# Performance work log

Measured on AMD Instinct MI355X. Metric: run time of the kernel, lower is better.

Reference implementation:

```python
import jax, jax.numpy as jnp
import numpy as np

D_MODEL = 1024
D_FFN = 4096
N_HEAD = 16
D_K = D_MODEL // N_HEAD
EPS = 1e-10


def _layernorm(x, gamma, beta):
    mean = jnp.mean(x, axis=-1, keepdims=True)
    var = jnp.mean((x - mean) ** 2, axis=-1, keepdims=True)
    return gamma * ((x - mean) / jnp.sqrt(var + EPS)) + beta


def setup_inputs() -> dict:
    key = jax.random.key(0)
    ks = jax.random.split(key, 16)
    s = 1.0 / np.sqrt(D_MODEL)
    sf = 1.0 / np.sqrt(D_FFN)
    return {
        "x": jax.random.normal(ks[0], (4, 2048, D_MODEL), jnp.float32),
        "wq": jax.random.uniform(ks[1], (D_MODEL, D_MODEL), jnp.float32, -s, s),
        "bq": jnp.zeros((D_MODEL,), jnp.float32),
        "wk": jax.random.uniform(ks[2], (D_MODEL, D_MODEL), jnp.float32, -s, s),
        "bk": jnp.zeros((D_MODEL,), jnp.float32),
        "wv": jax.random.uniform(ks[3], (D_MODEL, D_MODEL), jnp.float32, -s, s),
        "bv": jnp.zeros((D_MODEL,), jnp.float32),
        "wo": jax.random.uniform(ks[4], (D_MODEL, D_MODEL), jnp.float32, -s, s),
        "bo": jnp.zeros((D_MODEL,), jnp.float32),
        "g1": jnp.ones((D_MODEL,), jnp.float32),
        "b1": jnp.zeros((D_MODEL,), jnp.float32),
        "w1": jax.random.uniform(ks[5], (D_MODEL, D_FFN), jnp.float32, -s, s),
        "bf1": jnp.zeros((D_FFN,), jnp.float32),
        "w2": jax.random.uniform(ks[6], (D_FFN, D_MODEL), jnp.float32, -sf, sf),
        "bf2": jnp.zeros((D_MODEL,), jnp.float32),
        "g2": jnp.ones((D_MODEL,), jnp.float32),
        "b2": jnp.zeros((D_MODEL,), jnp.float32),
    }


def reference(x, wq, bq, wk, bk, wv, bv, wo, bo, g1, b1, w1, bf1, w2, bf2, g2, b2):
    B, S, _ = x.shape
    # projections -> (B, H, S, d_k)
    q = (x @ wq + bq).reshape(B, S, N_HEAD, D_K).transpose(0, 2, 1, 3)
    k = (x @ wk + bk).reshape(B, S, N_HEAD, D_K).transpose(0, 2, 1, 3)
    v = (x @ wv + bv).reshape(B, S, N_HEAD, D_K).transpose(0, 2, 1, 3)
    score = jnp.einsum("bhqd,bhkd->bhqk", q, k) / jnp.sqrt(jnp.asarray(D_K, x.dtype))
    attn = jax.nn.softmax(score, axis=-1)
    out = jnp.einsum("bhqk,bhkd->bhqd", attn, v)
    out = out.transpose(0, 2, 1, 3).reshape(B, S, D_MODEL)
    out = out @ wo + bo
    out1 = _layernorm(x + out, g1, b1)
    # FFN (dropout is identity in eval mode)
    ff = jax.nn.relu(out1 @ w1 + bf1) @ w2 + bf2
    out2 = _layernorm(out1 + ff, g2, b2)
    return (out2, attn)
```

## Files before the change

### kernel.cpp

```cpp
#include <hip/hip_runtime.h>
#include <hip/hip_bf16.h>

#define DEV __device__ __forceinline__

typedef __attribute__((ext_vector_type(4))) float f32x4;
typedef __attribute__((ext_vector_type(8))) __bf16 bf16v;
typedef __attribute__((ext_vector_type(8))) unsigned short u16x8;
typedef __attribute__((ext_vector_type(4))) unsigned short u16x4;

DEV unsigned short f2b(float x) {
    unsigned u = __builtin_bit_cast(unsigned, x);
    unsigned r = u + 0x7FFF + ((u >> 16) & 1);
    return (unsigned short)(r >> 16);
}

DEV void gl_lds16(const void* g, void* l) {
    __builtin_amdgcn_global_load_lds(
        (const __attribute__((address_space(1))) unsigned*)g,
        (__attribute__((address_space(3))) unsigned*)l,
        16, 0, 0);
}


__global__ __launch_bounds__(256) void cvt_f32_bf16(const float* __restrict__ in,
                                                    unsigned short* __restrict__ out, long n) {
    long i = ((long)blockIdx.x * 256 + threadIdx.x) * 4;
    if (i >= n) return;
    float4 f = *(const float4*)(in + i);
    u16x4 u;
    u[0] = f2b(f.x); u[1] = f2b(f.y); u[2] = f2b(f.z); u[3] = f2b(f.w);
    *(u16x4*)(out + i) = u;
}

__global__ __launch_bounds__(256) void transp_f32_bf16(const float* __restrict__ in,
                                                       unsigned short* __restrict__ out,
                                                       int R, int C) {
    __shared__ float t[32][33];
    int tx = threadIdx.x & 31, ty = threadIdx.x >> 5;
    long c0 = (long)blockIdx.x * 32, r0 = (long)blockIdx.y * 32;
#pragma unroll
    for (int i = 0; i < 4; i++)
        t[ty + i * 8][tx] = in[(r0 + ty + i * 8) * C + c0 + tx];
    __syncthreads();
#pragma unroll
    for (int i = 0; i < 4; i++)
        out[(c0 + ty + i * 8) * R + r0 + tx] = f2b(t[tx][ty + i * 8]);
}

DEV float waveSum(float v) {
#pragma unroll
    for (int o = 32; o > 0; o >>= 1) v += __shfl_xor(v, o);
    return v;
}

__global__ __launch_bounds__(256) void ln_rows(const float* __restrict__ in,
                                               const float* __restrict__ g,
                                               const float* __restrict__ b,
                                               float* __restrict__ outF,
                                               unsigned short* __restrict__ outB) {
    const float* p = in + (long)blockIdx.x * 1024;
    __shared__ float red[4], red2[4];
    int t = threadIdx.x, lane = t & 63, wave = t >> 6;
    float4 v = ((const float4*)p)[t];
    float s = v.x + v.y + v.z + v.w;
    float q = v.x * v.x + v.y * v.y + v.z * v.z + v.w * v.w;
    s = waveSum(s); q = waveSum(q);
    if (lane == 0) { red[wave] = s; red2[wave] = q; }
    __syncthreads();
    s = red[0] + red[1] + red[2] + red[3];
    q = red2[0] + red2[1] + red2[2] + red2[3];
    float mean = s * (1.0f / 1024.0f);
    float var = q * (1.0f / 1024.0f) - mean * mean;
    float rstd = rsqrtf(var + 1e-10f);
    float4 gg = ((const float4*)g)[t];
    float4 bb = ((const float4*)b)[t];
    float4 o;
    o.x = gg.x * ((v.x - mean) * rstd) + bb.x;
    o.y = gg.y * ((v.y - mean) * rstd) + bb.y;
    o.z = gg.z * ((v.z - mean) * rstd) + bb.z;
    o.w = gg.w * ((v.w - mean) * rstd) + bb.w;
    ((float4*)(outF + (long)blockIdx.x * 1024))[t] = o;
    if (outB) {
        u16x4 u;
        u[0] = f2b(o.x); u[1] = f2b(o.y); u[2] = f2b(o.z); u[3] = f2b(o.w);
        *(u16x4*)(outB + (long)blockIdx.x * 1024 + (long)t * 4) = u;
    }
}

__global__ __launch_bounds__(256, 2) void attn_fused(
    const unsigned short* __restrict__ qb,
    const unsigned short* __restrict__ kb,
    const unsigned short* __restrict__ vt,
    float* __restrict__ attn,
    unsigned short* __restrict__ ao) {
    __shared__ __align__(16) char smem[65536];
    __shared__ float sredM[4][16], sredS[4][16];

    int id = blockIdx.x;
    int swz = (id & 7) * 1024 + (id >> 3);
    const int z = swz >> 7;
    const int m0 = (swz & 127) * 16;

    const int tid = threadIdx.x, lane = tid & 63, w = tid >> 6;
    const int g = lane >> 4, l15 = lane & 15;

    const char* qz = (const char*)(qb + (long)z * 131072);
    const char* kz = (const char*)(kb + (long)z * 131072);
    const char* vz = (const char*)(vt + (long)z * 131072);

    const char* qrow = qz + (long)(m0 + l15) * 128;
    bf16v aq0 = *(const bf16v*)(qrow + g * 16);
    bf16v aq1 = *(const bf16v*)(qrow + 64 + g * 16);

    f32x4 acc[8][4];
#pragma unroll
    for (int c = 0; c < 8; c++)
#pragma unroll
        for (int t = 0; t < 4; t++) acc[c][t] = (f32x4)(0.0f);

    const int soff = ((lane & 7) * 16) ^ (((lane >> 3) & 7) << 4);

    for (int c = 0; c < 8; ++c) {
        const char* src = kz + (long)(c * 256 + w * 8 + (lane >> 3)) * 128 + soff;
#pragma unroll
        for (int i = 0; i < 8; ++i)
            gl_lds16(src + (long)i * 4096, smem + i * 4096 + w * 1024);
        __syncthreads();
#pragma unroll
        for (int t = 0; t < 4; ++t) {
            const int row = w * 64 + t * 16 + l15;
            const char* bp = smem + row * 128;
            const int sw = (lane & 7) << 4;
            bf16v bk0 = *(const bf16v*)(bp + ((g * 16) ^ sw));
            bf16v bk1 = *(const bf16v*)(bp + ((64 + g * 16) ^ sw));
            __builtin_amdgcn_s_setprio(1);
            acc[c][t] = __builtin_amdgcn_mfma_f32_16x16x32_bf16(aq0, bk0, acc[c][t], 0, 0, 0);
            acc[c][t] = __builtin_amdgcn_mfma_f32_16x16x32_bf16(aq1, bk1, acc[c][t], 0, 0, 0);
            __builtin_amdgcn_s_setprio(0);
        }
        __syncthreads();
    }

    float M[4], S[4];
#pragma unroll
    for (int j = 0; j < 4; ++j) {
        float m = -1e30f;
#pragma unroll
        for (int c = 0; c < 8; c++)
#pragma unroll
            for (int t = 0; t < 4; t++) m = fmaxf(m, acc[c][t][j]);
        m = fmaxf(m, __shfl_xor(m, 1));
        m = fmaxf(m, __shfl_xor(m, 2));
        m = fmaxf(m, __shfl_xor(m, 4));
        m = fmaxf(m, __shfl_xor(m, 8));
        M[j] = m;
    }
    if (l15 == 0) {
        sredM[w][g * 4 + 0] = M[0];
        sredM[w][g * 4 + 1] = M[1];
        sredM[w][g * 4 + 2] = M[2];
        sredM[w][g * 4 + 3] = M[3];
    }
    __syncthreads();
#pragma unroll
    for (int j = 0; j < 4; ++j) {
        int r = g * 4 + j;
        M[j] = 0.125f * fmaxf(fmaxf(sredM[0][r], sredM[1][r]),
                              fmaxf(sredM[2][r], sredM[3][r]));
        S[j] = 0.0f;
    }
#pragma unroll
    for (int c = 0; c < 8; c++)
#pragma unroll
        for (int t = 0; t < 4; t++) {
            f32x4 v = acc[c][t];
            v[0] = __expf(v[0] * 0.125f - M[0]);
            v[1] = __expf(v[1] * 0.125f - M[1]);
            v[2] = __expf(v[2] * 0.125f - M[2]);
            v[3] = __expf(v[3] * 0.125f - M[3]);
            acc[c][t] = v;
            S[0] += v[0]; S[1] += v[1]; S[2] += v[2]; S[3] += v[3];
        }
#pragma unroll
    for (int j = 0; j < 4; ++j) {
        float s = S[j];
        s += __shfl_xor(s, 1);
        s += __shfl_xor(s, 2);
        s += __shfl_xor(s, 4);
        s += __shfl_xor(s, 8);
        S[j] = s;
    }
    if (l15 == 0) {
        sredS[w][g * 4 + 0] = S[0];
        sredS[w][g * 4 + 1] = S[1];
        sredS[w][g * 4 + 2] = S[2];
        sredS[w][g * 4 + 3] = S[3];
    }
    __syncthreads();
    float inv[4];
#pragma unroll
    for (int j = 0; j < 4; ++j) {
        int r = g * 4 + j;
        inv[j] = 1.0f / (sredS[0][r] + sredS[1][r] + sredS[2][r] + sredS[3][r]);
    }

    float* ab = attn + (long)z * 4194304 + (long)m0 * 2048;
#pragma unroll
    for (int c = 0; c < 8; c++)
#pragma unroll
        for (int t = 0; t < 4; t++) {
            const int col = c * 256 + w * 64 + t * 16 + l15;
#pragma unroll
            for (int j = 0; j < 4; ++j) {
                const int r = g * 4 + j;
                float p = acc[c][t][j] * inv[j];
                ab[(long)r * 2048 + col] = p;
                *(unsigned short*)(smem + r * 4096 + ((col * 2) ^ ((r & 7) << 4))) = f2b(p);
            }
        }
    __syncthreads();

    f32x4 o0 = (f32x4)(0.0f), o1 = (f32x4)(0.0f);
    f32x4 o2 = (f32x4)(0.0f), o3 = (f32x4)(0.0f);
    const char* vtile = vz + (long)(w * 16 + l15) * 4096;
    const char* prow = smem + l15 * 4096;
    const int psw = (l15 & 7) << 4;
#pragma unroll 4
    for (int ks = 0; ks < 64; ks += 4) {
        bf16v pa0 = *(const bf16v*)(prow + (((ks + 0) * 64 + g * 16) ^ psw));
        bf16v pa1 = *(const bf16v*)(prow + (((ks + 1) * 64 + g * 16) ^ psw));
        bf16v pa2 = *(const bf16v*)(prow + (((ks + 2) * 64 + g * 16) ^ psw));
        bf16v pa3 = *(const bf16v*)(prow + (((ks + 3) * 64 + g * 16) ^ psw));
        bf16v bv0 = *(const bf16v*)(vtile + (ks + 0) * 64 + g * 16);
        bf16v bv1 = *(const bf16v*)(vtile + (ks + 1) * 64 + g * 16);
        bf16v bv2 = *(const bf16v*)(vtile + (ks + 2) * 64 + g * 16);
        bf16v bv3 = *(const bf16v*)(vtile + (ks + 3) * 64 + g * 16);
        __builtin_amdgcn_s_setprio(1);
        o0 = __builtin_amdgcn_mfma_f32_16x16x32_bf16(pa0, bv0, o0, 0, 0, 0);
        o1 = __builtin_amdgcn_mfma_f32_16x16x32_bf16(pa1, bv1, o1, 0, 0, 0);
        o2 = __builtin_amdgcn_mfma_f32_16x16x32_bf16(pa2, bv2, o2, 0, 0, 0);
        o3 = __builtin_amdgcn_mfma_f32_16x16x32_bf16(pa3, bv3, o3, 0, 0, 0);
        __builtin_amdgcn_s_setprio(0);
    }
    o0 = o0 + o1 + o2 + o3;

    const int b = z >> 4, h = z & 15;
    const long tokbase = (long)b * 2048 + m0 + g * 4;
#pragma unroll
    for (int j = 0; j < 4; ++j)
        ao[(tokbase + j) * 1024 + h * 64 + w * 16 + l15] = f2b(o0[j]);
}


enum { M_QKV3 = 0, M_RES = 1, M_RELU = 2 };

struct GArgs {
    const unsigned short* A;
    long lda;
    const unsigned short* B;
    long ldb;
    const float* bias;
    const float* resid;
    float* outF;
    unsigned short* outB;
    unsigned short* outB2;
    unsigned short* outB3;
    long ldo;
    int K;
};

template <int BM, int BN, int WR, int WC, int MODE>
__global__ __launch_bounds__(256) void gemm_k(GArgs g) {
    constexpr int MI = BM / (WR * 16), NI = BN / (WC * 16);
    __shared__ __align__(16) char sm[(BM + BN) * 128];
    char* sA = sm;
    char* sB = sm + BM * 128;
    const int tid = threadIdx.x, lane = tid & 63, wave = tid >> 6;
    const int wr = wave / WC, wc = wave % WC;
    const long m0 = (long)blockIdx.x * BM, n0 = (long)blockIdx.y * BN;

    const char* Ab = (const char*)(g.A + m0 * g.lda);
    const char* Bb = (const char*)(g.B + n0 * g.ldb);
    const long lda = g.lda, ldb = g.ldb;

    f32x4 acc[MI][NI];
#pragma unroll
    for (int mi = 0; mi < MI; mi++)
#pragma unroll
        for (int ni = 0; ni < NI; ni++) acc[mi][ni] = (f32x4)(0.0f);

    for (int k0 = 0; k0 < g.K; k0 += 64) {
#pragma unroll
        for (int i = 0; i < BM / 32; i++) {
            int c = i * 4 + wave;
            int p = c * 1024 + lane * 16;
            int row = p >> 7;
            int scb = (p & 127) ^ ((row & 7) << 4);
            gl_lds16(Ab + (long)row * (lda * 2) + (long)k0 * 2 + scb, sA + c * 1024);
        }
#pragma unroll
        for (int i = 0; i < BN / 32; i++) {
            int c = i * 4 + wave;
            int p = c * 1024 + lane * 16;
            int row = p >> 7;
            int scb = (p & 127) ^ ((row & 7) << 4);
            gl_lds16(Bb + (long)row * (ldb * 2) + (long)k0 * 2 + scb, sB + c * 1024);
        }
        __syncthreads();
#pragma unroll
        for (int ks = 0; ks < 2; ++ks) {
            const int cb = ks * 64 + (lane >> 4) * 16;
            bf16v af[MI], bfv[NI];
#pragma unroll
            for (int mi = 0; mi < MI; mi++) {
                int r = wr * (BM / WR) + mi * 16 + (lane & 15);
                af[mi] = *(const bf16v*)(sA + r * 128 + (cb ^ ((r & 7) << 4)));
            }
#pragma unroll
            for (int ni = 0; ni < NI; ni++) {
                int r = wc * (BN / WC) + ni * 16 + (lane & 15);
                bfv[ni] = *(const bf16v*)(sB + r * 128 + (cb ^ ((r & 7) << 4)));
            }
#pragma unroll
            for (int mi = 0; mi < MI; mi++)
#pragma unroll
                for (int ni = 0; ni < NI; ni++)
                    acc[mi][ni] = __builtin_amdgcn_mfma_f32_16x16x32_bf16(
                        af[mi], bfv[ni], acc[mi][ni], 0, 0, 0);
        }
        __syncthreads();
    }

#pragma unroll
    for (int mi = 0; mi < MI; mi++)
#pragma unroll
        for (int ni = 0; ni < NI; ni++) {
            if constexpr (MODE == M_QKV3) {
                long r = m0 + wr * (BM / WR) + mi * 16 + (lane >> 4) * 4;
                long c = n0 + wc * (BN / WC) + ni * 16 + (lane & 15);
                long b = r >> 11, s = r & 2047;
                float bi = g.bias[c];
                if (c < 2048) {
                    unsigned short* dst = (c < 1024) ? g.outB : g.outB2;
                    long h = (c >> 6) & 15, d = c & 63;
                    long base = ((b * 16 + h) * 2048 + s) * 64 + d;
#pragma unroll
                    for (int j = 0; j < 4; ++j)
                        dst[base + (long)j * 64] = f2b(acc[mi][ni][j] + bi);
                } else {
                    long h = (c - 2048) >> 6, d = c & 63;
                    u16x4 u;
#pragma unroll
                    for (int j = 0; j < 4; ++j) u[j] = f2b(acc[mi][ni][j] + bi);
                    *(u16x4*)(g.outB3 + (b * 16 + h) * 131072 + d * 2048 + s) = u;
                }
            } else {
#pragma unroll
                for (int j = 0; j < 4; ++j) {
                    long r = m0 + wr * (BM / WR) + mi * 16 + (lane >> 4) * 4 + j;
                    long c = n0 + wc * (BN / WC) + ni * 16 + (lane & 15);
                    float v = acc[mi][ni][j];
                    if constexpr (MODE == M_RES) {
                        long i = r * g.ldo + c;
                        g.outF[i] = v + g.bias[c] + g.resid[i];
                    } else {
                        float t = v + g.bias[c];
                        g.outB[r * g.ldo + c] = f2b(t > 0.0f ? t : 0.0f);
                    }
                }
            }
        }
}


extern "C" void kernel_launch(void* const* d_in, const int* in_sizes, int n_in,
                              void* d_out, int out_size, void* d_ws, size_t ws_size,
                              hipStream_t stream) {
    const float* x = (const float*)d_in[0];
    const float* wq = (const float*)d_in[1];
    const float* bq = (const float*)d_in[2];
    const float* wk = (const float*)d_in[3];
    const float* bk = (const float*)d_in[4];
    const float* wv = (const float*)d_in[5];
    const float* bv = (const float*)d_in[6];
    const float* wo = (const float*)d_in[7];
    const float* bo = (const float*)d_in[8];
    const float* g1 = (const float*)d_in[9];
    const float* b1 = (const float*)d_in[10];
    const float* w1 = (const float*)d_in[11];
    const float* bf1 = (const float*)d_in[12];
    const float* w2 = (const float*)d_in[13];
    const float* bf2 = (const float*)d_in[14];
    const float* g2 = (const float*)d_in[15];
    const float* b2 = (const float*)d_in[16];

    float* out2 = (float*)d_out;
    float* attn = (float*)d_out + 8388608;

    char* ws = (char*)d_ws;
    size_t off = 0;
    auto alc = [&](size_t bytes) { size_t r = off; off += (bytes + 255) & ~(size_t)255; return r; };

    unsigned short* xb    = (unsigned short*)(ws + alc(16777216));
    unsigned short* wqkvT = (unsigned short*)(ws + alc(6291456));
    unsigned short* woT   = (unsigned short*)(ws + alc(2097152));
    unsigned short* w1T   = (unsigned short*)(ws + alc(8388608));
    unsigned short* w2T   = (unsigned short*)(ws + alc(8388608));
    float* bqkv           = (float*)(ws + alc(12288));
    size_t bigOff = alc(67108864);
    unsigned short* qb = (unsigned short*)(ws + bigOff);
    unsigned short* kb = qb + 8388608;
    unsigned short* vt = kb + 8388608;
    unsigned short* ff1 = qb;
    size_t aoOff = alc(16777216);
    unsigned short* ao  = (unsigned short*)(ws + aoOff);
    unsigned short* o1b = ao;
    size_t rOff = alc(33554432);
    float* r1 = (float*)(ws + rOff);
    float* r2 = r1;
    float* o1f = (float*)(ws + alc(33554432));

    cvt_f32_bf16<<<8192, 256, 0, stream>>>(x, xb, 8388608);
    transp_f32_bf16<<<dim3(32, 32), 256, 0, stream>>>(wq, wqkvT, 1024, 1024);
    transp_f32_bf16<<<dim3(32, 32), 256, 0, stream>>>(wk, wqkvT + 1048576, 1024, 1024);
    transp_f32_bf16<<<dim3(32, 32), 256, 0, stream>>>(wv, wqkvT + 2097152, 1024, 1024);
    transp_f32_bf16<<<dim3(32, 32), 256, 0, stream>>>(wo, woT, 1024, 1024);
    transp_f32_bf16<<<dim3(128, 32), 256, 0, stream>>>(w1, w1T, 1024, 4096);
    transp_f32_bf16<<<dim3(32, 128), 256, 0, stream>>>(w2, w2T, 4096, 1024);
    hipMemcpyAsync(bqkv, bq, 4096, hipMemcpyDeviceToDevice, stream);
    hipMemcpyAsync(bqkv + 1024, bk, 4096, hipMemcpyDeviceToDevice, stream);
    hipMemcpyAsync(bqkv + 2048, bv, 4096, hipMemcpyDeviceToDevice, stream);

    {
        GArgs a{};
        a.A = xb; a.lda = 1024; a.B = wqkvT; a.ldb = 1024; a.K = 1024;
        a.bias = bqkv; a.outB = qb; a.outB2 = kb; a.outB3 = vt;
        gemm_k<128, 128, 2, 2, M_QKV3><<<dim3(64, 24), 256, 0, stream>>>(a);
    }
    attn_fused<<<8192, 256, 0, stream>>>(qb, kb, vt, attn, ao);
    {
        GArgs a{};
        a.A = ao; a.lda = 1024; a.B = woT; a.ldb = 1024;
        a.bias = bo; a.resid = x; a.outF = r1; a.ldo = 1024; a.K = 1024;
        gemm_k<128, 128, 2, 2, M_RES><<<dim3(64, 8), 256, 0, stream>>>(a);
    }
    ln_rows<<<8192, 256, 0, stream>>>(r1, g1, b1, o1f, o1b);
    {
        GArgs a{};
        a.A = o1b; a.lda = 1024; a.B = w1T; a.ldb = 1024;
        a.bias = bf1; a.outB = ff1; a.ldo = 4096; a.K = 1024;
        gemm_k<128, 128, 2, 2, M_RELU><<<dim3(64, 32), 256, 0, stream>>>(a);
    }
    {
        GArgs a{};
        a.A = ff1; a.lda = 4096; a.B = w2T; a.ldb = 4096;
        a.bias = bf2; a.resid = o1f; a.outF = r2; a.ldo = 1024; a.K = 4096;
        gemm_k<128, 128, 2, 2, M_RES><<<dim3(64, 8), 256, 0, stream>>>(a);
    }
    ln_rows<<<8192, 256, 0, stream>>>(r2, g2, b2, out2, nullptr);

    (void)in_sizes; (void)n_in; (void)out_size; (void)ws_size;
}
```

Baseline: 943.6 us.

## Merge prep kernels, use bf16 residual for FFN, drop MFMA setprio

The seven conversion and transpose launches and three memcpys are folded into one prep_all kernel to cut launch overhead. The first LayerNorm no longer writes its fp32 output, and the FFN down-projection reads its residual from the bf16 copy instead, removing a 32MB write and halving the residual read. It also removes s_setprio hints around the MFMAs in the attention kernel. Using the bf16 residual lowers precision in the second residual add.

```diff
diff --git a/kernel.cpp b/kernel.cpp
--- a/kernel.cpp
+++ b/kernel.cpp
@@ -12,6 +12,10 @@
     unsigned u = __builtin_bit_cast(unsigned, x);
     unsigned r = u + 0x7FFF + ((u >> 16) & 1);
     return (unsigned short)(r >> 16);
+}
+DEV float b2f(unsigned short u) {
+    unsigned v = (unsigned)u << 16;
+    return __builtin_bit_cast(float, v);
 }
 
 DEV void gl_lds16(const void* g, void* l) {
@@ -22,22 +26,10 @@
 }
 
 
-__global__ __launch_bounds__(256) void cvt_f32_bf16(const float* __restrict__ in,
-                                                    unsigned short* __restrict__ out, long n) {
-    long i = ((long)blockIdx.x * 256 + threadIdx.x) * 4;
-    if (i >= n) return;
-    float4 f = *(const float4*)(in + i);
-    u16x4 u;
-    u[0] = f2b(f.x); u[1] = f2b(f.y); u[2] = f2b(f.z); u[3] = f2b(f.w);
-    *(u16x4*)(out + i) = u;
-}
-
-__global__ __launch_bounds__(256) void transp_f32_bf16(const float* __restrict__ in,
-                                                       unsigned short* __restrict__ out,
-                                                       int R, int C) {
-    __shared__ float t[32][33];
+DEV void transp_dev(const float* __restrict__ in, unsigned short* __restrict__ out,
+                    int R, int C, int bx, int by, float (*t)[33]) {
     int tx = threadIdx.x & 31, ty = threadIdx.x >> 5;
-    long c0 = (long)blockIdx.x * 32, r0 = (long)blockIdx.y * 32;
+    long c0 = (long)bx * 32, r0 = (long)by * 32;
 #pragma unroll
     for (int i = 0; i < 4; i++)
         t[ty + i * 8][tx] = in[(r0 + ty + i * 8) * C + c0 + tx];
@@ -45,6 +37,43 @@
 #pragma unroll
     for (int i = 0; i < 4; i++)
         out[(c0 + ty + i * 8) * R + r0 + tx] = f2b(t[tx][ty + i * 8]);
+}
+
+__global__ __launch_bounds__(256) void prep_all(
+    const float* __restrict__ x, const float* __restrict__ wq,
+    const float* __restrict__ wk, const float* __restrict__ wv,
+    const float* __restrict__ wo, const float* __restrict__ w1,
+    const float* __restrict__ w2, const float* __restrict__ bq,
+    const float* __restrict__ bk, const float* __restrict__ bv,
+    unsigned short* __restrict__ xb, unsigned short* __restrict__ wqkvT,
+    unsigned short* __restrict__ woT, unsigned short* __restrict__ w1T,
+    unsigned short* __restrict__ w2T, float* __restrict__ bqkv) {
+    __shared__ float t[32][33];
+    int id = blockIdx.x;
+    if (id < 8192) {
+        long i = ((long)id * 256 + threadIdx.x) * 4;
+        float4 f = *(const float4*)(x + i);
+        u16x4 u;
+        u[0] = f2b(f.x); u[1] = f2b(f.y); u[2] = f2b(f.z); u[3] = f2b(f.w);
+        *(u16x4*)(xb + i) = u;
+        return;
+    }
+    id -= 8192;
+    if (id < 1024) { transp_dev(wq, wqkvT, 1024, 1024, id & 31, id >> 5, t); return; }
+    id -= 1024;
+    if (id < 1024) { transp_dev(wk, wqkvT + 1048576, 1024, 1024, id & 31, id >> 5, t); return; }
+    id -= 1024;
+    if (id < 1024) { transp_dev(wv, wqkvT + 2097152, 1024, 1024, id & 31, id >> 5, t); return; }
+    id -= 1024;
+    if (id < 1024) { transp_dev(wo, woT, 1024, 1024, id & 31, id >> 5, t); return; }
+    id -= 1024;
+    if (id < 4096) { transp_dev(w1, w1T, 1024, 4096, id & 127, id >> 7, t); return; }
+    id -= 4096;
+    if (id < 4096) { transp_dev(w2, w2T, 4096, 1024, id & 31, id >> 5, t); return; }
+    id -= 4096;
+    int i = id * 256 + threadIdx.x;
+    float v = (i < 1024) ? bq[i] : (i < 2048) ? bk[i - 1024] : bv[i - 2048];
+    bqkv[i] = v;
 }
 
 DEV float waveSum(float v) {
@@ -79,7 +108,7 @@
     o.y = gg.y * ((v.y - mean) * rstd) + bb.y;
     o.z = gg.z * ((v.z - mean) * rstd) + bb.z;
     o.w = gg.w * ((v.w - mean) * rstd) + bb.w;
-    ((float4*)(outF + (long)blockIdx.x * 1024))[t] = o;
+    if (outF) ((float4*)(outF + (long)blockIdx.x * 1024))[t] = o;
     if (outB) {
         u16x4 u;
         u[0] = f2b(o.x); u[1] = f2b(o.y); u[2] = f2b(o.z); u[3] = f2b(o.w);
@@ -133,10 +162,8 @@
             const int sw = (lane & 7) << 4;
             bf16v bk0 = *(const bf16v*)(bp + ((g * 16) ^ sw));
             bf16v bk1 = *(const bf16v*)(bp + ((64 + g * 16) ^ sw));
-            __builtin_amdgcn_s_setprio(1);
             acc[c][t] = __builtin_amdgcn_mfma_f32_16x16x32_bf16(aq0, bk0, acc[c][t], 0, 0, 0);
             acc[c][t] = __builtin_amdgcn_mfma_f32_16x16x32_bf16(aq1, bk1, acc[c][t], 0, 0, 0);
-            __builtin_amdgcn_s_setprio(0);
         }
         __syncthreads();
     }
@@ -235,12 +262,10 @@
         bf16v bv1 = *(const bf16v*)(vtile + (ks + 1) * 64 + g * 16);
         bf16v bv2 = *(const bf16v*)(vtile + (ks + 2) * 64 + g * 16);
         bf16v bv3 = *(const bf16v*)(vtile + (ks + 3) * 64 + g * 16);
-        __builtin_amdgcn_s_setprio(1);
         o0 = __builtin_amdgcn_mfma_f32_16x16x32_bf16(pa0, bv0, o0, 0, 0, 0);
         o1 = __builtin_amdgcn_mfma_f32_16x16x32_bf16(pa1, bv1, o1, 0, 0, 0);
         o2 = __builtin_amdgcn_mfma_f32_16x16x32_bf16(pa2, bv2, o2, 0, 0, 0);
         o3 = __builtin_amdgcn_mfma_f32_16x16x32_bf16(pa3, bv3, o3, 0, 0, 0);
-        __builtin_amdgcn_s_setprio(0);
     }
     o0 = o0 + o1 + o2 + o3;
 
@@ -252,7 +277,7 @@
 }
 
 
-enum { M_QKV3 = 0, M_RES = 1, M_RELU = 2 };
+enum { M_QKV3 = 0, M_RES = 1, M_RESB = 2, M_RELU = 3 };
 
 struct GArgs {
     const unsigned short* A;
@@ -261,6 +286,7 @@
     long ldb;
     const float* bias;
     const float* resid;
+    const unsigned short* residB;
     float* outF;
     unsigned short* outB;
     unsigned short* outB2;
@@ -363,6 +389,9 @@
                     if constexpr (MODE == M_RES) {
                         long i = r * g.ldo + c;
                         g.outF[i] = v + g.bias[c] + g.resid[i];
+                    } else if constexpr (MODE == M_RESB) {
+                        long i = r * g.ldo + c;
+                        g.outF[i] = v + g.bias[c] + b2f(g.residB[i]);
                     } else {
                         float t = v + g.bias[c];
                         g.outB[r * g.ldo + c] = f2b(t > 0.0f ? t : 0.0f);
@@ -418,18 +447,9 @@
     size_t rOff = alc(33554432);
     float* r1 = (float*)(ws + rOff);
     float* r2 = r1;
-    float* o1f = (float*)(ws + alc(33554432));
-
-    cvt_f32_bf16<<<8192, 256, 0, stream>>>(x, xb, 8388608);
-    transp_f32_bf16<<<dim3(32, 32), 256, 0, stream>>>(wq, wqkvT, 1024, 1024);
-    transp_f32_bf16<<<dim3(32, 32), 256, 0, stream>>>(wk, wqkvT + 1048576, 1024, 1024);
-    transp_f32_bf16<<<dim3(32, 32), 256, 0, stream>>>(wv, wqkvT + 2097152, 1024, 1024);
-    transp_f32_bf16<<<dim3(32, 32), 256, 0, stream>>>(wo, woT, 1024, 1024);
-    transp_f32_bf16<<<dim3(128, 32), 256, 0, stream>>>(w1, w1T, 1024, 4096);
-    transp_f32_bf16<<<dim3(32, 128), 256, 0, stream>>>(w2, w2T, 4096, 1024);
-    hipMemcpyAsync(bqkv, bq, 4096, hipMemcpyDeviceToDevice, stream);
-    hipMemcpyAsync(bqkv + 1024, bk, 4096, hipMemcpyDeviceToDevice, stream);
-    hipMemcpyAsync(bqkv + 2048, bv, 4096, hipMemcpyDeviceToDevice, stream);
+
+    prep_all<<<20492, 256, 0, stream>>>(x, wq, wk, wv, wo, w1, w2, bq, bk, bv,
+                                        xb, wqkvT, woT, w1T, w2T, bqkv);
 
     {
         GArgs a{};
@@ -444,7 +464,7 @@
         a.bias = bo; a.resid = x; a.outF = r1; a.ldo = 1024; a.K = 1024;
         gemm_k<128, 128, 2, 2, M_RES><<<dim3(64, 8), 256, 0, stream>>>(a);
     }
-    ln_rows<<<8192, 256, 0, stream>>>(r1, g1, b1, o1f, o1b);
+    ln_rows<<<8192, 256, 0, stream>>>(r1, g1, b1, nullptr, o1b);
     {
         GArgs a{};
         a.A = o1b; a.lda = 1024; a.B = w1T; a.ldb = 1024;
@@ -454,8 +474,8 @@
     {
         GArgs a{};
         a.A = ff1; a.lda = 4096; a.B = w2T; a.ldb = 4096;
-        a.bias = bf2; a.resid = o1f; a.outF = r2; a.ldo = 1024; a.K = 4096;
-        gemm_k<128, 128, 2, 2, M_RES><<<dim3(64, 8), 256, 0, stream>>>(a);
+        a.bias = bf2; a.residB = o1b; a.outF = r2; a.ldo = 1024; a.K = 4096;
+        gemm_k<128, 128, 2, 2, M_RESB><<<dim3(64, 8), 256, 0, stream>>>(a);
     }
     ln_rows<<<8192, 256, 0, stream>>>(r2, g2, b2, out2, nullptr);
 
```

New measurement: 906.3 us. -3.9%, faster.
